# Optimization experiments

Measured on AMD Instinct MI355X. Metric: run time of the kernel, lower is better.

Reference implementation:

```python
import jax, jax.numpy as jnp
import numpy as np

L, N, E, H, K = 2048, 8, 2048, 8192, 8

def setup_inputs() -> dict:
    key = jax.random.key(0)
    ks = jax.random.split(key, 6)
    return {
        'x': jax.random.normal(ks[0], (L, N, E), dtype=jnp.float32),
        'proj1': jax.random.normal(ks[1], (H, E), dtype=jnp.float32) * 0.02,
        'proj1_bias': jax.random.normal(ks[2], (H,), dtype=jnp.float32) * 0.02,
        'proj2': jax.random.normal(ks[3], (E, H), dtype=jnp.float32) * 0.02,
        'proj2_bias': jax.random.normal(ks[4], (E,), dtype=jnp.float32) * 0.02,
        'gate_w': jax.random.normal(ks[5], (E, K), dtype=jnp.float32),
    }

def reference(x, proj1, proj1_bias, proj2, proj2_bias, gate_w):
    # Gating: top-1 expert per token (argmax over expert affinities).
    # NOTE: in the source, every expert applies the SAME shared proj1/proj2,
    # and recv_from_experts restores the original token order exactly, so the
    # dispatch/combine is a mathematical identity permutation. The forward
    # math is therefore exactly a shared two-layer GELU MLP on all tokens.
    dst = jnp.argmax(jnp.einsum('lne,ek->lnk', x, gate_w), axis=-1)  # [L,N] int, routing ids
    h = jax.nn.gelu(jnp.einsum('lne,he->lnh', x, proj1) + proj1_bias, approximate=False)
    out = jnp.einsum('lnh,eh->lne', h, proj2) + proj2_bias
    del dst  # routing does not affect the output (shared expert weights)
    return out
```

## Files before the change

### kernel.cpp

```cpp
#include <hip/hip_runtime.h>
#include <hip/hip_bf16.h>
#include <cstdint>
#include <cstddef>

typedef __bf16 bf16_t;
typedef __bf16 bf16x4 __attribute__((ext_vector_type(4)));
typedef __bf16 bf16x8 __attribute__((ext_vector_type(8)));
typedef float  f32x4  __attribute__((ext_vector_type(4)));

#define L_DIM 2048
#define N_DIM 8
#define E_DIM 2048
#define H_DIM 8192
#define T_DIM (L_DIM * N_DIM)

__global__ __launch_bounds__(256) void cvt_f32_bf16(const float* __restrict__ in,
                                                    bf16_t* __restrict__ out,
                                                    int n4) {
    int stride = gridDim.x * blockDim.x;
    for (int i = blockIdx.x * blockDim.x + threadIdx.x; i < n4; i += stride) {
        float4 v = *(const float4*)(in + (size_t)i * 4);
        bf16x4 o;
        o[0] = (bf16_t)v.x; o[1] = (bf16_t)v.y;
        o[2] = (bf16_t)v.z; o[3] = (bf16_t)v.w;
        *(bf16x4*)(out + (size_t)i * 4) = o;
    }
}

__device__ __forceinline__ float fast_gelu(float x) {
    float x2 = x * x;
    float w  = x * __builtin_fmaf(0.1029456f, x2, 2.3022618f);
    w = fminf(w, 60.0f);
    float s = __builtin_amdgcn_exp2f(w);
    float r = __builtin_amdgcn_rcpf(s + 1.0f);
    return x * s * r;
}

template <bool GELU_OUT, int LG_NT, int LG_TN, int LG_NTILE, int KDIM, int NDIM>
__global__ __launch_bounds__(512, 2) void gemm256(const bf16_t* __restrict__ Am,
                                                  const bf16_t* __restrict__ Bm,
                                                  const float* __restrict__ bias,
                                                  void* __restrict__ Cout) {
    extern __shared__ char lds[];
    constexpr int NT    = 1 << LG_NT;
    constexpr int ntile = 1 << LG_NTILE;
    constexpr int U     = ntile << LG_NT;

    const int tid  = threadIdx.x;
    const int lane = tid & 63;
    const int wid  = tid >> 6;
    const int wr   = wid >> 2;
    const int wc   = wid & 3;

    const int wgb = (blockIdx.x & 7) * 32 + (blockIdx.x >> 3);
    const int g0  = wgb << LG_NTILE;

    const int srow  = wid * 8 + (lane >> 3);
    const int scol8 = ((lane & 7) ^ (lane >> 3)) * 8;

    auto STAGE = [&](int isB, int half, int slot) {
        const int us  = (slot < U) ? slot : (U - 1);
        const int ti_ = us >> LG_NT;
        const int kt_ = us & (NT - 1);
        const int g_  = g0 + ti_;
        const size_t base_ = (size_t)(isB ? (g_ & ((1 << LG_TN) - 1)) : (g_ >> LG_TN)) << 8;
        const unsigned reg_ = (unsigned)(((slot & 1) << 16) | (isB << 15) | (half << 14));
        const bf16_t* s0 = (isB ? Bm : Am)
                         + (base_ + (size_t)(half * 128 + srow)) * (size_t)KDIM
                         + (size_t)((kt_ << 6) + scol8);
        __builtin_amdgcn_global_load_lds(
            (const __attribute__((address_space(1))) void*)s0,
            (__attribute__((address_space(3))) void*)(lds + reg_ + (unsigned)(wid * 1024)),
            16, 0, 0);
        __builtin_amdgcn_global_load_lds(
            (const __attribute__((address_space(1))) void*)(s0 + (size_t)64 * KDIM),
            (__attribute__((address_space(3))) void*)(lds + reg_ + (unsigned)((8 + wid) * 1024)),
            16, 0, 0);
    };

    auto ldsA = [&](unsigned bufo, int m, int kk) -> bf16x8 {
        const int row  = (m >> 1) * 64 + wr * 32 + (m & 1) * 16 + (lane & 15);
        const int slot = ((kk << 2) + (lane >> 4)) ^ (lane & 7);
        return *(const bf16x8*)(lds + bufo + row * 128 + slot * 16);
    };
    auto ldsB = [&](unsigned bufo, int n, int kk) -> bf16x8 {
        const int row  = wc * 64 + n * 16 + (lane & 15);
        const int slot = ((kk << 2) + (lane >> 4)) ^ (lane & 7);
        return *(const bf16x8*)(lds + bufo + 32768 + row * 128 + slot * 16);
    };

    f32x4 acc[8][4] = {};

    STAGE(1, 0, 0); STAGE(1, 1, 0); STAGE(0, 0, 0); STAGE(0, 1, 0);
    asm volatile("s_waitcnt vmcnt(0)" ::: "memory");
    __builtin_amdgcn_s_barrier();

    for (int ti = 0; ti < ntile; ++ti) {
        for (int t = 0; t < NT; ++t) {
            const int u = (ti << LG_NT) + t;
            const unsigned cur = (unsigned)(t & 1) * 65536u;
            bf16x8 bf[4][2];
            bf16x8 af[2][2];

            STAGE(1, 0, u + 1);
#pragma unroll
            for (int n = 0; n < 4; ++n)
#pragma unroll
                for (int kk = 0; kk < 2; ++kk)
                    bf[n][kk] = ldsB(cur, n, kk);
#pragma unroll
            for (int mm = 0; mm < 2; ++mm)
#pragma unroll
                for (int kk = 0; kk < 2; ++kk)
                    af[mm][kk] = ldsA(cur, mm, kk);
            __builtin_amdgcn_s_barrier();
            asm volatile("s_waitcnt lgkmcnt(0)" ::: "memory");
            __builtin_amdgcn_s_setprio(1);
#pragma unroll
            for (int mm = 0; mm < 2; ++mm)
#pragma unroll
                for (int n = 0; n < 4; ++n)
#pragma unroll
                    for (int kk = 0; kk < 2; ++kk)
                        acc[mm][n] = __builtin_amdgcn_mfma_f32_16x16x32_bf16(
                            af[mm][kk], bf[n][kk], acc[mm][n], 0, 0, 0);
            __builtin_amdgcn_s_setprio(0);

            STAGE(1, 1, u + 1);
#pragma unroll
            for (int mm = 0; mm < 2; ++mm)
#pragma unroll
                for (int kk = 0; kk < 2; ++kk)
                    af[mm][kk] = ldsA(cur, 2 + mm, kk);
            asm volatile("s_waitcnt vmcnt(4)" ::: "memory");
            __builtin_amdgcn_s_barrier();
            asm volatile("s_waitcnt lgkmcnt(0)" ::: "memory");
            __builtin_amdgcn_s_setprio(1);
#pragma unroll
            for (int mm = 0; mm < 2; ++mm)
#pragma unroll
                for (int n = 0; n < 4; ++n)
#pragma unroll
                    for (int kk = 0; kk < 2; ++kk)
                        acc[2 + mm][n] = __builtin_amdgcn_mfma_f32_16x16x32_bf16(
                            af[mm][kk], bf[n][kk], acc[2 + mm][n], 0, 0, 0);
            __builtin_amdgcn_s_setprio(0);

            STAGE(0, 0, u + 1);
#pragma unroll
            for (int mm = 0; mm < 2; ++mm)
#pragma unroll
                for (int kk = 0; kk < 2; ++kk)
                    af[mm][kk] = ldsA(cur, 4 + mm, kk);
            __builtin_amdgcn_s_barrier();
            asm volatile("s_waitcnt lgkmcnt(0)" ::: "memory");
            __builtin_amdgcn_s_setprio(1);
#pragma unroll
            for (int mm = 0; mm < 2; ++mm)
#pragma unroll
                for (int n = 0; n < 4; ++n)
#pragma unroll
                    for (int kk = 0; kk < 2; ++kk)
                        acc[4 + mm][n] = __builtin_amdgcn_mfma_f32_16x16x32_bf16(
                            af[mm][kk], bf[n][kk], acc[4 + mm][n], 0, 0, 0);
            __builtin_amdgcn_s_setprio(0);

            STAGE(0, 1, u + 1);
#pragma unroll
            for (int mm = 0; mm < 2; ++mm)
#pragma unroll
                for (int kk = 0; kk < 2; ++kk)
                    af[mm][kk] = ldsA(cur, 6 + mm, kk);
            asm volatile("s_waitcnt vmcnt(2)" ::: "memory");
            __builtin_amdgcn_s_barrier();
            asm volatile("s_waitcnt lgkmcnt(0)" ::: "memory");
            __builtin_amdgcn_s_setprio(1);
#pragma unroll
            for (int mm = 0; mm < 2; ++mm)
#pragma unroll
                for (int n = 0; n < 4; ++n)
#pragma unroll
                    for (int kk = 0; kk < 2; ++kk)
                        acc[6 + mm][n] = __builtin_amdgcn_mfma_f32_16x16x32_bf16(
                            af[mm][kk], bf[n][kk], acc[6 + mm][n], 0, 0, 0);
            __builtin_amdgcn_s_setprio(0);
        }

        const int g = g0 + ti;
        const size_t rowBase = (size_t)(g >> LG_TN) << 8;
        const size_t colBase = (size_t)(g & ((1 << LG_TN) - 1)) << 8;
        const int orow = (lane >> 4) * 4;
        const int ocol = lane & 15;
#pragma unroll
        for (int m = 0; m < 8; ++m) {
            const size_t rb = rowBase + (size_t)((m >> 1) * 64 + wr * 32 + (m & 1) * 16 + orow);
#pragma unroll
            for (int n = 0; n < 4; ++n) {
                const size_t col = colBase + (size_t)(wc * 64 + n * 16 + ocol);
                const float bv = bias[col];
#pragma unroll
                for (int j = 0; j < 4; ++j) {
                    float v = acc[m][n][j] + bv;
                    if constexpr (GELU_OUT) {
                        ((bf16_t*)Cout)[(rb + j) * (size_t)NDIM + col] = (bf16_t)fast_gelu(v);
                    } else {
                        ((float*)Cout)[(rb + j) * (size_t)NDIM + col] = v;
                    }
                }
                acc[m][n] = (f32x4){0.f, 0.f, 0.f, 0.f};
            }
        }
    }
    asm volatile("s_waitcnt vmcnt(0)" ::: "memory");
}

extern "C" void kernel_launch(void* const* d_in, const int* in_sizes, int n_in,
                              void* d_out, int out_size, void* d_ws, size_t ws_size,
                              hipStream_t stream) {
    const float* x  = (const float*)d_in[0];
    const float* p1 = (const float*)d_in[1];
    const float* b1 = (const float*)d_in[2];
    const float* p2 = (const float*)d_in[3];
    const float* b2 = (const float*)d_in[4];
    float* out = (float*)d_out;

    char* ws = (char*)d_ws;
    bf16_t* xb  = (bf16_t*)(ws);
    bf16_t* p1b = (bf16_t*)(ws + ((size_t)64 << 20));
    bf16_t* p2b = (bf16_t*)(ws + ((size_t)96 << 20));
    bf16_t* h   = (bf16_t*)(ws + ((size_t)128 << 20));

    auto g1 = gemm256<true, 5, 5, 3, E_DIM, H_DIM>;
    auto g2 = gemm256<false, 7, 3, 1, H_DIM, E_DIM>;

    (void)hipFuncSetAttribute((const void*)g1,
                              hipFuncAttributeMaxDynamicSharedMemorySize, 131072);
    (void)hipFuncSetAttribute((const void*)g2,
                              hipFuncAttributeMaxDynamicSharedMemorySize, 131072);

    cvt_f32_bf16<<<2048, 256, 0, stream>>>(x,  xb,  (T_DIM * E_DIM) / 4);
    cvt_f32_bf16<<<1024, 256, 0, stream>>>(p1, p1b, (H_DIM * E_DIM) / 4);
    cvt_f32_bf16<<<1024, 256, 0, stream>>>(p2, p2b, (E_DIM * H_DIM) / 4);

    g1<<<256, 512, 131072, stream>>>(xb, p1b, b1, (void*)h);
    g2<<<256, 512, 131072, stream>>>(h, p2b, b2, (void*)out);
}
```

Baseline: 1.019 ms.

## Reschedule GEMM pipeline barriers and use a non-persistent deeper-prefetch kernel for the second GEMM

```diff
diff --git a/kernel.cpp b/kernel.cpp
--- a/kernel.cpp
+++ b/kernel.cpp
@@ -102,18 +102,18 @@
             bf16x8 bf[4][2];
             bf16x8 af[2][2];
 
+#pragma unroll
+            for (int n = 0; n < 4; ++n)
+#pragma unroll
+                for (int kk = 0; kk < 2; ++kk)
+                    bf[n][kk] = ldsB(cur, n, kk);
+#pragma unroll
+            for (int mm = 0; mm < 2; ++mm)
+#pragma unroll
+                for (int kk = 0; kk < 2; ++kk)
+                    af[mm][kk] = ldsA(cur, mm, kk);
             STAGE(1, 0, u + 1);
-#pragma unroll
-            for (int n = 0; n < 4; ++n)
-#pragma unroll
-                for (int kk = 0; kk < 2; ++kk)
-                    bf[n][kk] = ldsB(cur, n, kk);
-#pragma unroll
-            for (int mm = 0; mm < 2; ++mm)
-#pragma unroll
-                for (int kk = 0; kk < 2; ++kk)
-                    af[mm][kk] = ldsA(cur, mm, kk);
-            __builtin_amdgcn_s_barrier();
+            STAGE(1, 1, u + 1);
             asm volatile("s_waitcnt lgkmcnt(0)" ::: "memory");
             __builtin_amdgcn_s_setprio(1);
 #pragma unroll
@@ -125,34 +125,32 @@
                         acc[mm][n] = __builtin_amdgcn_mfma_f32_16x16x32_bf16(
                             af[mm][kk], bf[n][kk], acc[mm][n], 0, 0, 0);
             __builtin_amdgcn_s_setprio(0);
-
-            STAGE(1, 1, u + 1);
 #pragma unroll
             for (int mm = 0; mm < 2; ++mm)
 #pragma unroll
                 for (int kk = 0; kk < 2; ++kk)
                     af[mm][kk] = ldsA(cur, 2 + mm, kk);
+            asm volatile("s_waitcnt lgkmcnt(0)" ::: "memory");
+            __builtin_amdgcn_s_setprio(1);
+#pragma unroll
+            for (int mm = 0; mm < 2; ++mm)
+#pragma unroll
+                for (int n = 0; n < 4; ++n)
+#pragma unroll
+                    for (int kk = 0; kk < 2; ++kk)
+                        acc[2 + mm][n] = __builtin_amdgcn_mfma_f32_16x16x32_bf16(
+                            af[mm][kk], bf[n][kk], acc[2 + mm][n], 0, 0, 0);
+            __builtin_amdgcn_s_setprio(0);
             asm volatile("s_waitcnt vmcnt(4)" ::: "memory");
             __builtin_amdgcn_s_barrier();
-            asm volatile("s_waitcnt lgkmcnt(0)" ::: "memory");
-            __builtin_amdgcn_s_setprio(1);
-#pragma unroll
-            for (int mm = 0; mm < 2; ++mm)
-#pragma unroll
-                for (int n = 0; n < 4; ++n)
-#pragma unroll
-                    for (int kk = 0; kk < 2; ++kk)
-                        acc[2 + mm][n] = __builtin_amdgcn_mfma_f32_16x16x32_bf16(
-                            af[mm][kk], bf[n][kk], acc[2 + mm][n], 0, 0, 0);
-            __builtin_amdgcn_s_setprio(0);
-
+
+#pragma unroll
+            for (int mm = 0; mm < 2; ++mm)
+#pragma unroll
+                for (int kk = 0; kk < 2; ++kk)
+                    af[mm][kk] = ldsA(cur, 4 + mm, kk);
             STAGE(0, 0, u + 1);
-#pragma unroll
-            for (int mm = 0; mm < 2; ++mm)
-#pragma unroll
-                for (int kk = 0; kk < 2; ++kk)
-                    af[mm][kk] = ldsA(cur, 4 + mm, kk);
-            __builtin_amdgcn_s_barrier();
+            STAGE(0, 1, u + 1);
             asm volatile("s_waitcnt lgkmcnt(0)" ::: "memory");
             __builtin_amdgcn_s_setprio(1);
 #pragma unroll
@@ -164,26 +162,24 @@
                         acc[4 + mm][n] = __builtin_amdgcn_mfma_f32_16x16x32_bf16(
                             af[mm][kk], bf[n][kk], acc[4 + mm][n], 0, 0, 0);
             __builtin_amdgcn_s_setprio(0);
-
-            STAGE(0, 1, u + 1);
 #pragma unroll
             for (int mm = 0; mm < 2; ++mm)
 #pragma unroll
                 for (int kk = 0; kk < 2; ++kk)
                     af[mm][kk] = ldsA(cur, 6 + mm, kk);
+            asm volatile("s_waitcnt lgkmcnt(0)" ::: "memory");
+            __builtin_amdgcn_s_setprio(1);
+#pragma unroll
+            for (int mm = 0; mm < 2; ++mm)
+#pragma unroll
+                for (int n = 0; n < 4; ++n)
+#pragma unroll
+                    for (int kk = 0; kk < 2; ++kk)
+                        acc[6 + mm][n] = __builtin_amdgcn_mfma_f32_16x16x32_bf16(
+                            af[mm][kk], bf[n][kk], acc[6 + mm][n], 0, 0, 0);
+            __builtin_amdgcn_s_setprio(0);
             asm volatile("s_waitcnt vmcnt(2)" ::: "memory");
             __builtin_amdgcn_s_barrier();
-            asm volatile("s_waitcnt lgkmcnt(0)" ::: "memory");
-            __builtin_amdgcn_s_setprio(1);
-#pragma unroll
-            for (int mm = 0; mm < 2; ++mm)
-#pragma unroll
-                for (int n = 0; n < 4; ++n)
-#pragma unroll
-                    for (int kk = 0; kk < 2; ++kk)
-                        acc[6 + mm][n] = __builtin_amdgcn_mfma_f32_16x16x32_bf16(
-                            af[mm][kk], bf[n][kk], acc[6 + mm][n], 0, 0, 0);
-            __builtin_amdgcn_s_setprio(0);
         }
 
         const int g = g0 + ti;
@@ -214,6 +210,146 @@
     asm volatile("s_waitcnt vmcnt(0)" ::: "memory");
 }
 
+template <bool GELU_OUT>
+__global__ __launch_bounds__(512, 2) void gemm256_p8(const bf16_t* __restrict__ Am,
+                                                     const bf16_t* __restrict__ Bm,
+                                                     const float* __restrict__ bias,
+                                                     void* __restrict__ Cout,
+                                                     int M, int N, int K) {
+    extern __shared__ char lds[];
+    const int NT = K / 64;
+
+    const int tid  = threadIdx.x;
+    const int lane = tid & 63;
+    const int wid  = tid >> 6;
+    const int wr   = wid >> 2;
+    const int wc   = wid & 3;
+
+    const int nTn = N / 256;
+    const int nwg = (M / 256) * nTn;
+    const int q   = nwg >> 3;
+    const int wg  = (blockIdx.x & 7) * q + (blockIdx.x >> 3);
+    const size_t rowBase = (size_t)(wg / nTn) * 256;
+    const size_t colBase = (size_t)(wg % nTn) * 256;
+
+    const int srow  = wid * 8 + (lane >> 3);
+    const int scol8 = ((lane & 7) ^ (lane >> 3)) * 8;
+
+    auto STAGE = [&](int isB, int half, int slot) {
+        const int kt_ = (slot < NT) ? slot : (NT - 1);
+        const unsigned reg_ = (unsigned)((slot & 1) * 65536 + isB * 32768 + half * 16384);
+        const bf16_t* gbase_ = isB ? Bm : Am;
+        const size_t gr_ = (isB ? colBase : rowBase) + (size_t)(half * 128 + srow);
+        const bf16_t* s0 = gbase_ + gr_ * (size_t)K + (size_t)(kt_ * 64 + scol8);
+        __builtin_amdgcn_global_load_lds(
+            (const __attribute__((address_space(1))) void*)s0,
+            (__attribute__((address_space(3))) void*)(lds + reg_ + (unsigned)(wid * 1024)),
+            16, 0, 0);
+        __builtin_amdgcn_global_load_lds(
+            (const __attribute__((address_space(1))) void*)(s0 + (size_t)64 * K),
+            (__attribute__((address_space(3))) void*)(lds + reg_ + (unsigned)((8 + wid) * 1024)),
+            16, 0, 0);
+    };
+
+    auto ldsA = [&](unsigned bufo, int m, int kk) -> bf16x8 {
+        const int row  = (m >> 1) * 64 + wr * 32 + (m & 1) * 16 + (lane & 15);
+        const int slot = ((kk << 2) + (lane >> 4)) ^ (lane & 7);
+        return *(const bf16x8*)(lds + bufo + row * 128 + slot * 16);
+    };
+    auto ldsB = [&](unsigned bufo, int n, int kk) -> bf16x8 {
+        const int row  = wc * 64 + n * 16 + (lane & 15);
+        const int slot = ((kk << 2) + (lane >> 4)) ^ (lane & 7);
+        return *(const bf16x8*)(lds + bufo + 32768 + row * 128 + slot * 16);
+    };
+
+    f32x4 acc[8][4] = {};
+
+    STAGE(1, 0, 0); STAGE(1, 1, 0); STAGE(0, 0, 0); STAGE(0, 1, 0);
+    STAGE(1, 0, 1); STAGE(1, 1, 1); STAGE(0, 0, 1);
+    asm volatile("s_waitcnt vmcnt(6)" ::: "memory");
+    __builtin_amdgcn_s_barrier();
+
+    for (int t = 0; t < NT; ++t) {
+        const unsigned cur = (unsigned)(t & 1) * 65536u;
+        bf16x8 bf[4][2];
+        bf16x8 af[2][2];
+
+#pragma unroll
+        for (int n = 0; n < 4; ++n)
+#pragma unroll
+            for (int kk = 0; kk < 2; ++kk)
+                bf[n][kk] = ldsB(cur, n, kk);
+#pragma unroll
+        for (int mm = 0; mm < 2; ++mm)
+#pragma unroll
+            for (int kk = 0; kk < 2; ++kk)
+                af[mm][kk] = ldsA(cur, mm, kk);
+        STAGE(0, 1, t + 1);
+        asm volatile("s_waitcnt lgkmcnt(8)" ::: "memory");
+        __builtin_amdgcn_s_barrier();
+        asm volatile("s_waitcnt lgkmcnt(0)" ::: "memory");
+        __builtin_amdgcn_s_setprio(1);
+#pragma unroll
+        for (int mm = 0; mm < 2; ++mm)
+#pragma unroll
+            for (int n = 0; n < 4; ++n)
+#pragma unroll
+                for (int kk = 0; kk < 2; ++kk)
+                    acc[mm][n] = __builtin_amdgcn_mfma_f32_16x16x32_bf16(
+                        af[mm][kk], bf[n][kk], acc[mm][n], 0, 0, 0);
+        __builtin_amdgcn_s_setprio(0);
+        __builtin_amdgcn_s_barrier();
+
+#pragma unroll
+        for (int ph = 1; ph < 4; ++ph) {
+#pragma unroll
+            for (int mm = 0; mm < 2; ++mm)
+#pragma unroll
+                for (int kk = 0; kk < 2; ++kk)
+                    af[mm][kk] = ldsA(cur, ph * 2 + mm, kk);
+            if (ph == 1)      STAGE(1, 0, t + 2);
+            else if (ph == 2) STAGE(1, 1, t + 2);
+            else {            STAGE(0, 0, t + 2);
+                              asm volatile("s_waitcnt vmcnt(6)" ::: "memory"); }
+            __builtin_amdgcn_s_barrier();
+            asm volatile("s_waitcnt lgkmcnt(0)" ::: "memory");
+            __builtin_amdgcn_s_setprio(1);
+#pragma unroll
+            for (int mm = 0; mm < 2; ++mm)
+#pragma unroll
+                for (int n = 0; n < 4; ++n)
+#pragma unroll
+                    for (int kk = 0; kk < 2; ++kk)
+                        acc[ph * 2 + mm][n] = __builtin_amdgcn_mfma_f32_16x16x32_bf16(
+                            af[mm][kk], bf[n][kk], acc[ph * 2 + mm][n], 0, 0, 0);
+            __builtin_amdgcn_s_setprio(0);
+            __builtin_amdgcn_s_barrier();
+        }
+    }
+    asm volatile("s_waitcnt vmcnt(0)" ::: "memory");
+
+    const int orow = (lane >> 4) * 4;
+    const int ocol = lane & 15;
+#pragma unroll
+    for (int m = 0; m < 8; ++m) {
+        const size_t rb = rowBase + (size_t)((m >> 1) * 64 + wr * 32 + (m & 1) * 16 + orow);
+#pragma unroll
+        for (int n = 0; n < 4; ++n) {
+            const size_t col = colBase + (size_t)(wc * 64 + n * 16 + ocol);
+            const float bv = bias[col];
+#pragma unroll
+            for (int j = 0; j < 4; ++j) {
+                float v = acc[m][n][j] + bv;
+                if constexpr (GELU_OUT) {
+                    ((bf16_t*)Cout)[(rb + j) * (size_t)N + col] = (bf16_t)fast_gelu(v);
+                } else {
+                    ((float*)Cout)[(rb + j) * (size_t)N + col] = v;
+                }
+            }
+        }
+    }
+}
+
 extern "C" void kernel_launch(void* const* d_in, const int* in_sizes, int n_in,
                               void* d_out, int out_size, void* d_ws, size_t ws_size,
                               hipStream_t stream) {
@@ -231,7 +367,7 @@
     bf16_t* h   = (bf16_t*)(ws + ((size_t)128 << 20));
 
     auto g1 = gemm256<true, 5, 5, 3, E_DIM, H_DIM>;
-    auto g2 = gemm256<false, 7, 3, 1, H_DIM, E_DIM>;
+    auto g2 = gemm256_p8<false>;
 
     (void)hipFuncSetAttribute((const void*)g1,
                               hipFuncAttributeMaxDynamicSharedMemorySize, 131072);
@@ -243,5 +379,6 @@
     cvt_f32_bf16<<<1024, 256, 0, stream>>>(p2, p2b, (E_DIM * H_DIM) / 4);
 
     g1<<<256, 512, 131072, stream>>>(xb, p1b, b1, (void*)h);
-    g2<<<256, 512, 131072, stream>>>(h, p2b, b2, (void*)out);
-}
+    g2<<<(T_DIM / 256) * (E_DIM / 256), 512, 131072, stream>>>(
+        h, p2b, b2, (void*)out, T_DIM, E_DIM, H_DIM);
+}
```

Result: no change. 1.012 ms (-0.7%).
